# Kernel optimization log

Hardware: AMD Instinct MI355X
Metric: run time of the kernel (lower is better)

Reference implementation:

```python
import jax, jax.numpy as jnp
import numpy as np

B, F, T = 4, 2048, 2048
CF, CT = 1024, 1024
H, DH = 16, 64
ALPHA = 1.0 / np.sqrt(DH).astype(np.float32)


def setup_inputs() -> dict:
    key = jax.random.key(0)
    ks = jax.random.split(key, 8)
    s = 0.02  # trunc_normal-ish init scale
    return {
        "from_tensor": jax.random.normal(ks[0], (B, F, CF), jnp.float32),
        "to_tensor": jax.random.normal(ks[1], (B, T, CT), jnp.float32),
        "mask": jax.random.randint(ks[2], (B, F, T), 0, 2, jnp.int32),
        "Wq": jax.random.normal(ks[3], (CF, H * DH), jnp.float32) * s,
        "bq": jnp.zeros((H * DH,), jnp.float32),
        "Wk": jax.random.normal(ks[4], (CT, H * DH), jnp.float32) * s,
        "bk": jnp.zeros((H * DH,), jnp.float32),
        "Wv": jax.random.normal(ks[5], (CT, H * DH), jnp.float32) * s,
        "bv": jnp.zeros((H * DH,), jnp.float32),
    }


def reference(from_tensor, to_tensor, mask, Wq, bq, Wk, bk, Wv, bv):
    # projections (nn.Linear with no activation)
    q = from_tensor @ Wq + bq          # [B,F,H*DH]
    k = to_tensor @ Wk + bk            # [B,T,H*DH]
    v = to_tensor @ Wv + bv            # [B,T,H*DH]
    q = q.reshape(B, F, H, DH)         # query: [..., F, H, DH]
    k = k.reshape(B, T, DH, H)         # key:   [..., T, DH, H]  (self._shape[::-1])
    v = v.reshape(B, T, H, DH)
    # score = transpose(q,-3,-2) @ transpose(k,-3,-1) * alpha -> [B,H,F,T]
    score = jnp.einsum("bfhd,btdh->bhft", q, k) * ALPHA
    if mask is not None:
        adder = (1.0 - mask[:, None].astype(score.dtype)) * -100000.0  # [B,1,F,T]
        score = score + adder
    probs = jax.nn.softmax(score, axis=-1)  # dropout p=0.0 -> identity
    # context = probs @ transpose(v,-3,-2), then transpose back: [B,F,H,DH]
    context = jnp.einsum("bhft,bthd->bfhd", probs, v)
    return context.reshape(B, F, H * DH)
```

## Files before the change

kernel.cpp:

```cpp
#include <hip/hip_runtime.h>
#include <type_traits>

typedef __bf16 bf16_t;
typedef __attribute__((ext_vector_type(8))) __bf16 bf16x8;
typedef __attribute__((ext_vector_type(4))) float f32x4;
typedef __attribute__((ext_vector_type(16))) float f32x16;

__device__ __forceinline__ void async16(const void* g, void* lds) {
  __builtin_amdgcn_global_load_lds((const __attribute__((address_space(1))) unsigned int*)g,
                                   (__attribute__((address_space(3))) unsigned int*)lds, 16, 0, 0);
}

__device__ __forceinline__ unsigned pk2(float lo, float hi) {
  unsigned short a = __builtin_bit_cast(unsigned short, (__bf16)lo);
  unsigned short b = __builtin_bit_cast(unsigned short, (__bf16)hi);
  return (unsigned)a | ((unsigned)b << 16);
}

__device__ __forceinline__ void plswap(unsigned& a, unsigned& b) {
#if __has_builtin(__builtin_amdgcn_permlane32_swap)
  auto r = __builtin_amdgcn_permlane32_swap((int)a, (int)b, false, false);
  a = (unsigned)r[0];
  b = (unsigned)r[1];
#else
  const bool hb = (threadIdx.x & 32) != 0;
  unsigned bx = (unsigned)__shfl_xor((int)b, 32);
  unsigned ax = (unsigned)__shfl_xor((int)a, 32);
  unsigned na = hb ? bx : a;
  unsigned nb = hb ? b : ax;
  a = na; b = nb;
#endif
}

__global__ __launch_bounds__(256) void prep_kernel(const int* __restrict__ mask, unsigned long long* __restrict__ mb,
                                                   const float* __restrict__ Wq, const float* __restrict__ Wk,
                                                   const float* __restrict__ Wv, bf16_t* __restrict__ Wt,
                                                   const float* __restrict__ from, bf16_t* __restrict__ inbF,
                                                   const float* __restrict__ to_, bf16_t* __restrict__ inbT) {
  const int bid = blockIdx.x, tid = threadIdx.x;
  if (bid < 2048) {
    const int lane = tid & 63, w = tid >> 6;
    for (int i = 0; i < 32; ++i) {
      size_t word = (size_t)bid * 128 + (size_t)i * 4 + w;
      unsigned long long bits = __ballot(mask[word * 64 + lane] != 0);
      if (lane == 0) mb[word] = bits;
    }
  } else if (bid < 3584) {
    const int idx = bid - 2048;
    const int z = idx >> 9, r = idx & 511;
    const float* src = (z == 0) ? Wq : ((z == 1) ? Wk : Wv);
    const float sc = (z == 0) ? 0.18033688011112042f : 1.0f;
    bf16_t* dst = Wt + (size_t)z * 1024 * 1024;
    const int n = (r & 15) * 64 + (tid & 63);
    const int k8 = (r >> 4) * 4 + (tid >> 6);
    bf16x8 o;
#pragma unroll
    for (int j = 0; j < 8; ++j) o[j] = (__bf16)(src[(size_t)(k8 * 8 + j) * 1024 + n] * sc);
    *(bf16x8*)(dst + (size_t)n * 1024 + k8 * 8) = o;
  } else {
    const bool isF = bid < 7680;
    const size_t i = (size_t)(bid - (isF ? 3584 : 7680)) * 256 + tid;
    const float4* in4 = (const float4*)(isF ? from : to_);
    bf16_t* outp = isF ? inbF : inbT;
    float4 a = in4[i * 2], b = in4[i * 2 + 1];
    bf16x8 o;
    o[0] = (__bf16)a.x; o[1] = (__bf16)a.y; o[2] = (__bf16)a.z; o[3] = (__bf16)a.w;
    o[4] = (__bf16)b.x; o[5] = (__bf16)b.y; o[6] = (__bf16)b.z; o[7] = (__bf16)b.w;
    *(bf16x8*)(outp + i * 8) = o;
  }
}

__global__ __launch_bounds__(256) void proj_kernel(const bf16_t* __restrict__ inbF, const bf16_t* __restrict__ inbT,
                                                   const bf16_t* __restrict__ Wt,
                                                   const float* __restrict__ bq, const float* __restrict__ bk,
                                                   const float* __restrict__ bv,
                                                   bf16_t* __restrict__ Qw, bf16_t* __restrict__ Kw,
                                                   bf16_t* __restrict__ Vw) {
  __shared__ __align__(16) unsigned char smem[33792];
  bf16_t* se = (bf16_t*)smem;
  const int z = blockIdx.z;
  const bf16_t* A = (z == 0) ? inbF : inbT;
  const bf16_t* Wz = Wt + (size_t)z * 1024 * 1024;
  const float* bias = (z == 0) ? bq : ((z == 1) ? bk : bv);
  bf16_t* dst = (z == 0) ? Qw : ((z == 1) ? Kw : Vw);
  const float bscale = (z == 0) ? 0.18033688011112042f : 1.0f;

  const int tid = threadIdx.x, lane = tid & 63, w = tid >> 6;
  const int m0 = blockIdx.x * 128, n0 = blockIdx.y * 128;
  const int wm = (w >> 1) * 64, wn = (w & 1) * 64;
  const int r = lane & 15, kq = lane >> 4;
  const int srow = lane >> 2, sslot = lane & 3;
  f32x4 acc[4][4] = {};

  auto stage = [&](int buf, int k0) {
    bf16_t* Ad = se + buf * 4096;
    bf16_t* Bd = se + 8192 + buf * 4096;
#pragma unroll
    for (int it = 0; it < 2; ++it) {
      const int c = it * 4 + w;
      const int row = c * 16 + srow;
      async16(A + (size_t)(m0 + row) * 1024 + k0 + ((sslot ^ (row & 3)) * 8), Ad + c * 512);
      async16(Wz + (size_t)(n0 + row) * 1024 + k0 + ((sslot ^ (row & 3)) * 8), Bd + c * 512);
    }
  };

  stage(0, 0);
  __syncthreads();
  for (int tile = 0; tile < 32; ++tile) {
    const int cur = tile & 1;
    if (tile < 31) stage(cur ^ 1, (tile + 1) * 32);
    const bf16_t* Al = se + cur * 4096;
    const bf16_t* Bl = se + 8192 + cur * 4096;
    bf16x8 af[4], bfr[4];
#pragma unroll
    for (int i = 0; i < 4; ++i) {
      const int ra = wm + i * 16 + r;
      af[i] = *(const bf16x8*)(Al + ra * 32 + ((kq ^ (ra & 3)) * 8));
      const int rb = wn + i * 16 + r;
      bfr[i] = *(const bf16x8*)(Bl + rb * 32 + ((kq ^ (rb & 3)) * 8));
    }
    __builtin_amdgcn_s_setprio(1);
#pragma unroll
    for (int i = 0; i < 4; ++i)
#pragma unroll
      for (int j = 0; j < 4; ++j)
        acc[i][j] = __builtin_amdgcn_mfma_f32_16x16x32_bf16(af[i], bfr[j], acc[i][j], 0, 0, 0);
    __builtin_amdgcn_s_setprio(0);
    __syncthreads();
  }

  bf16_t* Cl = se;
  float bvv[4];
#pragma unroll
  for (int j = 0; j < 4; ++j) bvv[j] = bias[n0 + wn + j * 16 + r] * bscale;
#pragma unroll
  for (int i = 0; i < 4; ++i)
#pragma unroll
    for (int j = 0; j < 4; ++j)
#pragma unroll
      for (int g = 0; g < 4; ++g)
        Cl[(wm + i * 16 + kq * 4 + g) * 132 + wn + j * 16 + r] = (__bf16)(acc[i][j][g] + bvv[j]);
  __syncthreads();

  const int b = m0 >> 11, sbase = m0 & 2047;
  if (z == 0) {
#pragma unroll
    for (int q = 0; q < 8; ++q) {
      const int cid = q * 256 + tid;
      const int m = cid >> 4, c = (cid >> 3) & 1, d8 = cid & 7;
      bf16x8 val = *(const bf16x8*)(Cl + m * 132 + c * 64 + d8 * 8);
      *(bf16x8*)(dst + ((size_t)(b * 16 + (n0 >> 6) + c) * 2048 + sbase + m) * 64 + d8 * 8) = val;
    }
  } else if (z == 1) {
#pragma unroll
    for (int q = 0; q < 8; ++q) {
      const int cid = q * 256 + tid;
      const int hh = cid >> 7, m = cid & 127;
      bf16x8 val;
#pragma unroll
      for (int dd = 0; dd < 8; ++dd) val[dd] = Cl[m * 132 + dd * 16 + hh];
      *(bf16x8*)(dst + ((size_t)(b * 16 + hh) * 2048 + sbase + m) * 64 + (n0 >> 4)) = val;
    }
  } else {
#pragma unroll
    for (int q = 0; q < 8; ++q) {
      const int cid = q * 256 + tid;
      const int nl = cid >> 4, m8 = cid & 15;
      bf16x8 val;
#pragma unroll
      for (int s = 0; s < 8; ++s) val[s] = Cl[(m8 * 8 + s) * 132 + nl];
      const int hh = (n0 >> 6) + (nl >> 6), dd = nl & 63;
      *(bf16x8*)(dst + ((size_t)(b * 16 + hh) * 64 + dd) * 2048 + sbase + m8 * 8) = val;
    }
  }
}

__global__ __launch_bounds__(256, 2) void attn_kernel(const bf16_t* __restrict__ Q, const bf16_t* __restrict__ K,
                                                      const bf16_t* __restrict__ VT,
                                                      const unsigned long long* __restrict__ mb,
                                                      float* __restrict__ out) {
  __shared__ __align__(16) unsigned char smem[32768];
  bf16_t* se = (bf16_t*)smem;
  const int tid = threadIdx.x, lane = tid & 63, w = tid >> 6;
  const int cl = lane & 31, hi = lane >> 5;

  const int lid = blockIdx.x + 8 * (blockIdx.y + 16 * blockIdx.z);
  const int xcd = lid & 7, q_ = lid >> 3;
  const int pairIdx = xcd * 8 + (q_ & 7);
  const int f0 = (q_ >> 3) * 256;
  const int h = pairIdx & 15, b = pairIdx >> 4;

  const size_t bh = (size_t)b * 16 + h;
  const int fw = f0 + w * 64;

  const bf16_t* Qb = Q + (bh * 2048 + fw) * 64;
  bf16x8 qf[2][4];
#pragma unroll
  for (int fb = 0; fb < 2; ++fb)
#pragma unroll
    for (int ks = 0; ks < 4; ++ks)
      qf[fb][ks] = *(const bf16x8*)(Qb + (fb * 32 + cl) * 64 + ks * 16 + hi * 8);

  f32x16 Of[2][2] = {};
  float lacc[2] = {0.f, 0.f};
  bf16x8 paw[2][4];

  const unsigned long long* mrow[2];
  mrow[0] = mb + ((size_t)b * 2048 + fw + cl) * 32;
  mrow[1] = mb + ((size_t)b * 2048 + fw + 32 + cl) * 32;

  const int row8 = lane >> 3, slot = lane & 7;
  const int swz = (slot ^ row8) * 8;
  const bf16_t* kgb[2];
  const bf16_t* vgb[2];
#pragma unroll
  for (int it = 0; it < 2; ++it) {
    const int row = it * 32 + w * 8 + row8;
    kgb[it] = K + (bh * 2048 + row) * 64 + swz;
    vgb[it] = VT + (bh * 64 + row) * 2048 + swz;
  }

  auto stage_k = [&](int buf, int tile) {
    bf16_t* kd = se + buf * 4096 + w * 512;
#pragma unroll
    for (int it = 0; it < 2; ++it)
      async16(kgb[it] + (size_t)tile * 4096, kd + it * 2048);
  };
  auto stage_v = [&](int buf, int tile) {
    bf16_t* vd = se + 8192 + buf * 4096 + w * 512;
#pragma unroll
    for (int it = 0; it < 2; ++it)
      async16(vgb[it] + (size_t)tile * 64, vd + it * 2048);
  };

  auto pv_step = [&](int vbuf) {
    const bf16_t* Vl = se + 8192 + vbuf * 4096;
    __builtin_amdgcn_s_setprio(1);
#pragma unroll
    for (int db = 0; db < 2; ++db) {
      const int vrow0 = db * 32 + cl;
#pragma unroll
      for (int kt = 0; kt < 4; ++kt) {
        bf16x8 vf = *(const bf16x8*)(Vl + vrow0 * 64 + (((2 * kt + hi) ^ (vrow0 & 7)) * 8));
        Of[0][db] = __builtin_amdgcn_mfma_f32_32x32x16_bf16(paw[0][kt], vf, Of[0][db], 0, 0, 0);
        Of[1][db] = __builtin_amdgcn_mfma_f32_32x32x16_bf16(paw[1][kt], vf, Of[1][db], 0, 0, 0);
      }
    }
    __builtin_amdgcn_s_setprio(0);
  };

  unsigned long long mA[2], mB[2];
  stage_k(0, 0);
  mA[0] = mrow[0][0];
  mA[1] = mrow[1][0];
  __syncthreads();

  auto body = [&](auto curc, auto dopvc, unsigned long long (&mc)[2], unsigned long long (&mn)[2], int tile) {
    constexpr int cur = decltype(curc)::value;
    constexpr bool dopv = decltype(dopvc)::value;
    if (tile < 31) {
      stage_k(cur ^ 1, tile + 1);
      mn[0] = mrow[0][tile + 1];
      mn[1] = mrow[1][tile + 1];
    }
    stage_v(cur, tile);
    const bf16_t* Kl = se + cur * 4096;

    f32x16 st0[2], st1[2];
#pragma unroll
    for (int fb = 0; fb < 2; ++fb) {
      const unsigned mw0 = (unsigned)(mc[fb] >> (4 * hi));
      const unsigned mw1 = (unsigned)(mc[fb] >> (32 + 4 * hi));
#pragma unroll
      for (int q = 0; q < 4; ++q)
#pragma unroll
        for (int e = 0; e < 4; ++e) {
          const int idx = q * 4 + e;
          const int pos = e + 8 * q;
          const unsigned s0 = (unsigned)(((int)(mw0 << (31 - pos))) >> 31);
          const unsigned s1 = (unsigned)(((int)(mw1 << (31 - pos))) >> 31);
          st0[fb][idx] = __uint_as_float(~s0 & 0xC6EA6000u);
          st1[fb][idx] = __uint_as_float(~s1 & 0xC6EA6000u);
        }
    }

    {
      const int krow = cl;
      __builtin_amdgcn_s_setprio(1);
#pragma unroll
      for (int ks = 0; ks < 4; ++ks) {
        bf16x8 kf = *(const bf16x8*)(Kl + krow * 64 + (((2 * ks + hi) ^ (krow & 7)) * 8));
        st0[0] = __builtin_amdgcn_mfma_f32_32x32x16_bf16(kf, qf[0][ks], st0[0], 0, 0, 0);
        st0[1] = __builtin_amdgcn_mfma_f32_32x32x16_bf16(kf, qf[1][ks], st0[1], 0, 0, 0);
      }
      __builtin_amdgcn_s_setprio(0);
    }

    if constexpr (dopv) pv_step(cur ^ 1);

    {
      const int krow = 32 + cl;
      __builtin_amdgcn_s_setprio(1);
#pragma unroll
      for (int ks = 0; ks < 4; ++ks) {
        bf16x8 kf = *(const bf16x8*)(Kl + krow * 64 + (((2 * ks + hi) ^ (krow & 7)) * 8));
        st1[0] = __builtin_amdgcn_mfma_f32_32x32x16_bf16(kf, qf[0][ks], st1[0], 0, 0, 0);
        st1[1] = __builtin_amdgcn_mfma_f32_32x32x16_bf16(kf, qf[1][ks], st1[1], 0, 0, 0);
      }
      __builtin_amdgcn_s_setprio(0);
    }

#pragma unroll
    for (int ts = 0; ts < 2; ++ts) {
#pragma unroll
      for (int fb = 0; fb < 2; ++fb) {
        const f32x16& stf = (ts == 0) ? st0[fb] : st1[fb];
        float pv[16];
#pragma unroll
        for (int q = 0; q < 4; ++q)
#pragma unroll
          for (int e = 0; e < 4; ++e) {
            const int idx = q * 4 + e;
            float p = __builtin_amdgcn_exp2f(stf[idx]);
            lacc[fb] += p;
            pv[idx] = p;
          }
#pragma unroll
        for (int kl = 0; kl < 2; ++kl) {
          const int qa = 2 * kl, qb = qa + 1;
          unsigned x0 = pk2(pv[qa * 4 + 0], pv[qa * 4 + 1]);
          unsigned y0 = pk2(pv[qb * 4 + 0], pv[qb * 4 + 1]);
          unsigned x1 = pk2(pv[qa * 4 + 2], pv[qa * 4 + 3]);
          unsigned y1 = pk2(pv[qb * 4 + 2], pv[qb * 4 + 3]);
          plswap(x0, y0);
          plswap(x1, y1);
          union { unsigned u[4]; bf16x8 v; } tmp;
          tmp.u[0] = x0; tmp.u[1] = x1; tmp.u[2] = y0; tmp.u[3] = y1;
          paw[fb][ts * 2 + kl] = tmp.v;
        }
      }
    }
    __syncthreads();
  };

  using c0 = std::integral_constant<int, 0>;
  using c1 = std::integral_constant<int, 1>;
  using bF = std::integral_constant<bool, false>;
  using bT = std::integral_constant<bool, true>;

  body(c0{}, bF{}, mA, mB, 0);
  body(c1{}, bT{}, mB, mA, 1);
  for (int tile = 2; tile < 32; tile += 2) {
    body(c0{}, bT{}, mA, mB, tile);
    body(c1{}, bT{}, mB, mA, tile + 1);
  }
  pv_step(1);

#pragma unroll
  for (int fb = 0; fb < 2; ++fb) lacc[fb] += __shfl_xor(lacc[fb], 32);
  float* lsh = (float*)smem;
  if (hi == 0) {
    lsh[w * 64 + cl] = lacc[0];
    lsh[w * 64 + 32 + cl] = lacc[1];
  }
#pragma unroll
  for (int fb = 0; fb < 2; ++fb)
#pragma unroll
    for (int q = 0; q < 4; ++q)
#pragma unroll
      for (int e = 0; e < 4; ++e) {
        const int idx = q * 4 + e;
        const int row = e + 8 * q + 4 * hi;
        const float li = 1.0f / lsh[w * 64 + fb * 32 + row];
        const size_t orow = ((size_t)b * 2048 + fw + fb * 32 + row) * 1024 + h * 64;
        out[orow + cl] = Of[fb][0][idx] * li;
        out[orow + 32 + cl] = Of[fb][1][idx] * li;
      }
}

extern "C" void kernel_launch(void* const* d_in, const int* in_sizes, int n_in,
                              void* d_out, int out_size, void* d_ws, size_t ws_size,
                              hipStream_t stream) {
  (void)in_sizes; (void)n_in; (void)out_size; (void)ws_size;
  const float* from = (const float*)d_in[0];
  const float* to_  = (const float*)d_in[1];
  const int*   mask = (const int*)d_in[2];
  const float* Wq = (const float*)d_in[3];
  const float* bq = (const float*)d_in[4];
  const float* Wk = (const float*)d_in[5];
  const float* bk = (const float*)d_in[6];
  const float* Wv = (const float*)d_in[7];
  const float* bv = (const float*)d_in[8];
  float* out = (float*)d_out;
  char* ws = (char*)d_ws;

  bf16_t* Qw = (bf16_t*)(ws);
  bf16_t* Kw = (bf16_t*)(ws + (size_t)(1u << 24));
  bf16_t* Vw = (bf16_t*)(ws + (size_t)(2u << 24));
  bf16_t* Wt = (bf16_t*)(ws + (size_t)(3u << 24));
  unsigned long long* mbits = (unsigned long long*)(ws + (size_t)(3u << 24) + (size_t)(6u << 20));
  bf16_t* inbF = (bf16_t*)(ws + (size_t)(3u << 24) + (size_t)(8u << 20));
  bf16_t* inbT = (bf16_t*)d_out;

  prep_kernel<<<11776, 256, 0, stream>>>(mask, mbits, Wq, Wk, Wv, Wt, from, inbF, to_, inbT);
  proj_kernel<<<dim3(64, 8, 3), 256, 0, stream>>>(inbF, inbT, Wt, bq, bk, bv, Qw, Kw, Vw);
  attn_kernel<<<dim3(8, 16, 4), 256, 0, stream>>>(Qw, Kw, Vw, mbits, out);
}
```

Measured before the change: 204.1 us.

## Split attention over key halves with partial outputs and a reduction kernel

Each (batch, head, query-block) attention block now processes only half of the key sequence. This doubles the grid to 1024 blocks, and each block writes unnormalized partial outputs and row sums. A separate reduce kernel adds the two partials and divides by the combined sum. The intent is more parallelism and better load balance, at the cost of extra fp32 partial traffic, a second launch, and a larger workspace footprint.

```diff
diff --git a/kernel.cpp b/kernel.cpp
--- a/kernel.cpp
+++ b/kernel.cpp
@@ -175,23 +175,28 @@
   }
 }
 
-__global__ __launch_bounds__(256, 2) void attn_kernel(const bf16_t* __restrict__ Q, const bf16_t* __restrict__ K,
-                                                      const bf16_t* __restrict__ VT,
-                                                      const unsigned long long* __restrict__ mb,
-                                                      float* __restrict__ out) {
+__global__ __launch_bounds__(256, 2) void attn_part_kernel(const bf16_t* __restrict__ Q, const bf16_t* __restrict__ K,
+                                                           const bf16_t* __restrict__ VT,
+                                                           const unsigned long long* __restrict__ mb,
+                                                           float* __restrict__ Op0, float* __restrict__ Op1,
+                                                           float* __restrict__ Lp) {
   __shared__ __align__(16) unsigned char smem[32768];
   bf16_t* se = (bf16_t*)smem;
   const int tid = threadIdx.x, lane = tid & 63, w = tid >> 6;
   const int cl = lane & 31, hi = lane >> 5;
 
-  const int lid = blockIdx.x + 8 * (blockIdx.y + 16 * blockIdx.z);
+  const int lid = blockIdx.x;
   const int xcd = lid & 7, q_ = lid >> 3;
   const int pairIdx = xcd * 8 + (q_ & 7);
-  const int f0 = (q_ >> 3) * 256;
+  const int rest = q_ >> 3;
+  const int f0 = (rest & 7) * 256;
+  const int half = rest >> 3;
+  const int tbase = half * 16;
   const int h = pairIdx & 15, b = pairIdx >> 4;
 
   const size_t bh = (size_t)b * 16 + h;
   const int fw = f0 + w * 64;
+  float* Ob = half ? Op1 : Op0;
 
   const bf16_t* Qb = Q + (bh * 2048 + fw) * 64;
   bf16x8 qf[2][4];
@@ -206,8 +211,8 @@
   bf16x8 paw[2][4];
 
   const unsigned long long* mrow[2];
-  mrow[0] = mb + ((size_t)b * 2048 + fw + cl) * 32;
-  mrow[1] = mb + ((size_t)b * 2048 + fw + 32 + cl) * 32;
+  mrow[0] = mb + ((size_t)b * 2048 + fw + cl) * 32 + tbase;
+  mrow[1] = mb + ((size_t)b * 2048 + fw + 32 + cl) * 32 + tbase;
 
   const int row8 = lane >> 3, slot = lane & 7;
   const int swz = (slot ^ row8) * 8;
@@ -216,8 +221,8 @@
 #pragma unroll
   for (int it = 0; it < 2; ++it) {
     const int row = it * 32 + w * 8 + row8;
-    kgb[it] = K + (bh * 2048 + row) * 64 + swz;
-    vgb[it] = VT + (bh * 64 + row) * 2048 + swz;
+    kgb[it] = K + (bh * 2048 + (size_t)tbase * 64 + row) * 64 + swz;
+    vgb[it] = VT + (bh * 64 + row) * 2048 + (size_t)tbase * 64 + swz;
   }
 
   auto stage_k = [&](int buf, int tile) {
@@ -258,7 +263,7 @@
   auto body = [&](auto curc, auto dopvc, unsigned long long (&mc)[2], unsigned long long (&mn)[2], int tile) {
     constexpr int cur = decltype(curc)::value;
     constexpr bool dopv = decltype(dopvc)::value;
-    if (tile < 31) {
+    if (tile < 15) {
       stage_k(cur ^ 1, tile + 1);
       mn[0] = mrow[0][tile + 1];
       mn[1] = mrow[1][tile + 1];
@@ -350,7 +355,7 @@
 
   body(c0{}, bF{}, mA, mB, 0);
   body(c1{}, bT{}, mB, mA, 1);
-  for (int tile = 2; tile < 32; tile += 2) {
+  for (int tile = 2; tile < 16; tile += 2) {
     body(c0{}, bT{}, mA, mB, tile);
     body(c1{}, bT{}, mB, mA, tile + 1);
   }
@@ -358,10 +363,10 @@
 
 #pragma unroll
   for (int fb = 0; fb < 2; ++fb) lacc[fb] += __shfl_xor(lacc[fb], 32);
-  float* lsh = (float*)smem;
   if (hi == 0) {
-    lsh[w * 64 + cl] = lacc[0];
-    lsh[w * 64 + 32 + cl] = lacc[1];
+#pragma unroll
+    for (int fb = 0; fb < 2; ++fb)
+      Lp[(size_t)half * 131072 + bh * 2048 + fw + fb * 32 + cl] = lacc[fb];
   }
 #pragma unroll
   for (int fb = 0; fb < 2; ++fb)
@@ -371,11 +376,24 @@
       for (int e = 0; e < 4; ++e) {
         const int idx = q * 4 + e;
         const int row = e + 8 * q + 4 * hi;
-        const float li = 1.0f / lsh[w * 64 + fb * 32 + row];
         const size_t orow = ((size_t)b * 2048 + fw + fb * 32 + row) * 1024 + h * 64;
-        out[orow + cl] = Of[fb][0][idx] * li;
-        out[orow + 32 + cl] = Of[fb][1][idx] * li;
+        Ob[orow + cl] = Of[fb][0][idx];
+        Ob[orow + 32 + cl] = Of[fb][1][idx];
       }
+}
+
+__global__ __launch_bounds__(256) void attn_reduce_kernel(float* __restrict__ Op0, const float* __restrict__ Op1,
+                                                          const float* __restrict__ Lp) {
+  const size_t i4 = ((size_t)blockIdx.x * 256 + threadIdx.x) * 4;
+  const size_t rowd = i4 >> 6;
+  const int hh = (int)(rowd & 15);
+  const size_t bf = rowd >> 4;
+  const int bb = (int)(bf >> 11);
+  const size_t lidx = ((size_t)bb * 16 + hh) * 2048 + (bf & 2047);
+  const float li = 1.0f / (Lp[lidx] + Lp[131072 + lidx]);
+  f32x4 a = *(const f32x4*)(Op0 + i4);
+  f32x4 c = *(const f32x4*)(Op1 + i4);
+  *(f32x4*)(Op0 + i4) = (a + c) * li;
 }
 
 extern "C" void kernel_launch(void* const* d_in, const int* in_sizes, int n_in,
@@ -399,10 +417,14 @@
   bf16_t* Vw = (bf16_t*)(ws + (size_t)(2u << 24));
   bf16_t* Wt = (bf16_t*)(ws + (size_t)(3u << 24));
   unsigned long long* mbits = (unsigned long long*)(ws + (size_t)(3u << 24) + (size_t)(6u << 20));
-  bf16_t* inbF = (bf16_t*)(ws + (size_t)(3u << 24) + (size_t)(8u << 20));
+  float* Op1 = (float*)(ws + (size_t)(3u << 24) + (size_t)(8u << 20));
+  float* Lp  = (float*)(ws + (size_t)(3u << 24) + (size_t)(8u << 20) + ((size_t)1 << 25));
   bf16_t* inbT = (bf16_t*)d_out;
+  bf16_t* inbF = (bf16_t*)((char*)d_out + (1u << 24));
+  float* Op0 = out;
 
   prep_kernel<<<11776, 256, 0, stream>>>(mask, mbits, Wq, Wk, Wv, Wt, from, inbF, to_, inbT);
   proj_kernel<<<dim3(64, 8, 3), 256, 0, stream>>>(inbF, inbT, Wt, bq, bk, bv, Qw, Kw, Vw);
-  attn_kernel<<<dim3(8, 16, 4), 256, 0, stream>>>(Qw, Kw, Vw, mbits, out);
-}
+  attn_part_kernel<<<1024, 256, 0, stream>>>(Qw, Kw, Vw, mbits, Op0, Op1, Lp);
+  attn_reduce_kernel<<<8192, 256, 0, stream>>>(Op0, Op1, Lp);
+}
```

Result: slower. 226.9 us (+11.2%).
